# Kernel tuning notes

Hardware: AMD Instinct MI355X
Metric: run time of the kernel (lower is better)

The kernel has to match this reference:

```python
import jax, jax.numpy as jnp
import numpy as np
import math

NUM_WORDS = 8192
WORD_WIDTH = 512
PROJ_WIDTH = 64
NUM_HEADS = 8
SCALE_FACTOR = 100.0

def setup_inputs() -> dict:
    key = jax.random.key(0)
    kx, kq, kk, kv, ko = jax.random.split(key, 5)
    x = jax.random.normal(kx, (NUM_WORDS, WORD_WIDTH), dtype=jnp.float32)
    w_q = jax.random.normal(kq, (WORD_WIDTH, PROJ_WIDTH), dtype=jnp.float32) / SCALE_FACTOR
    w_k = jax.random.normal(kk, (WORD_WIDTH, PROJ_WIDTH), dtype=jnp.float32) / SCALE_FACTOR
    w_v = jax.random.normal(kv, (WORD_WIDTH, PROJ_WIDTH), dtype=jnp.float32) / SCALE_FACTOR
    w_o = jax.random.normal(ko, (WORD_WIDTH, WORD_WIDTH), dtype=jnp.float32)
    return {"x": x, "w_q": w_q, "w_k": w_k, "w_v": w_v, "w_o": w_o}

def reference(x, w_q, w_k, w_v, w_o):
    # Single self-attention head (all 8 heads in the source share the same weights).
    q = x @ w_q            # [N, P]
    k = x @ w_k            # [N, P]
    v = x @ w_v            # [N, P]
    scores = jax.nn.softmax((q @ k.T) / jnp.sqrt(jnp.float32(q.shape[1])), axis=1)  # [N, N]
    head = scores @ v      # [N, P]
    # concat of NUM_HEADS identical head outputs along dim=1
    concat = jnp.tile(head, (1, NUM_HEADS))  # [N, NUM_HEADS*P]
    return concat @ w_o    # [N, WORD_WIDTH]
```

## Files before the change

kernel.cpp:

```cpp
#include <hip/hip_runtime.h>
#include <stdint.h>

#define N_WORDS 8192
#define LOG2E_8 0.18033688011112043f

typedef __attribute__((ext_vector_type(8))) short short8;
typedef __attribute__((ext_vector_type(4))) float f32x4;
typedef __attribute__((ext_vector_type(2))) __fp16 pkhalf2;
typedef __attribute__((ext_vector_type(4))) _Float16 half4;
typedef __attribute__((ext_vector_type(8))) _Float16 half8;

__device__ __forceinline__ unsigned short f32_to_bf16(float f) {
    union { float f; unsigned u; } v; v.f = f;
    unsigned u = v.u;
    return (unsigned short)((u + 0x7FFFu + ((u >> 16) & 1u)) >> 16);
}

__device__ __forceinline__ unsigned short f32_to_f16(float f) {
    union { _Float16 h; unsigned short u; } cv;
    cv.h = (_Float16)f;
    return cv.u;
}

__device__ __forceinline__ void async16(const void* g, void* l) {
    __builtin_amdgcn_global_load_lds(
        (const __attribute__((address_space(1))) unsigned int*)g,
        (__attribute__((address_space(3))) unsigned int*)l, 16, 0, 0);
}

__global__ __launch_bounds__(256) void qkv_gemm(
    const float* __restrict__ x,
    const float* __restrict__ wq, const float* __restrict__ wk,
    const float* __restrict__ wv, const float* __restrict__ wo,
    unsigned short* __restrict__ qB, unsigned short* __restrict__ kB,
    unsigned short* __restrict__ vH, unsigned short* __restrict__ weT)
{
    int t = threadIdx.x;
    int mat = blockIdx.y;

    if (mat == 3) {
        int i = blockIdx.x * 256 + t;
        int p = i >> 9;
        int j = i & 511;
        float s = 0.0f;
#pragma unroll
        for (int h = 0; h < 8; ++h) s += wo[(size_t)(h * 64 + p) * 512 + j];
        weT[(size_t)j * 64 + p] = f32_to_f16(s);
        return;
    }

    __shared__ __align__(16) unsigned short ldsX[64 * 72];
    __shared__ __align__(16) unsigned short ldsW[64 * 72];

    int mt = blockIdx.x;
    const float* w = (mat == 0) ? wq : (mat == 1) ? wk : wv;

    int wvid = t >> 6, lane = t & 63;
    int lq = lane & 15, quad = lane >> 4;

    f32x4 acc[4];
#pragma unroll
    for (int nt = 0; nt < 4; ++nt) acc[nt] = (f32x4){0.f, 0.f, 0.f, 0.f};

    float4 xr[4];
    float wr[16];
    int wn = t & 63, wkbs = (t >> 6) * 16;

    {
        int k0 = 0;
#pragma unroll
        for (int j2 = 0; j2 < 4; ++j2) {
            int i = t + j2 * 256;
            int row = i >> 4, c4 = (i & 15) * 4;
            xr[j2] = *(const float4*)(x + (size_t)(mt * 64 + row) * 512 + k0 + c4);
        }
#pragma unroll
        for (int kk = 0; kk < 16; ++kk)
            wr[kk] = w[(size_t)(k0 + wkbs + kk) * 64 + wn];
    }

    for (int kb = 0; kb < 8; ++kb) {
        __syncthreads();
#pragma unroll
        for (int j2 = 0; j2 < 4; ++j2) {
            int i = t + j2 * 256;
            int row = i >> 4, c4 = (i & 15) * 4;
            unsigned p0 = f32_to_bf16(xr[j2].x) | ((unsigned)f32_to_bf16(xr[j2].y) << 16);
            unsigned p1 = f32_to_bf16(xr[j2].z) | ((unsigned)f32_to_bf16(xr[j2].w) << 16);
            *(uint2*)(&ldsX[row * 72 + c4]) = make_uint2(p0, p1);
        }
#pragma unroll
        for (int kk = 0; kk < 16; kk += 2) {
            unsigned p = f32_to_bf16(wr[kk]) | ((unsigned)f32_to_bf16(wr[kk + 1]) << 16);
            *(unsigned*)(&ldsW[wn * 72 + wkbs + kk]) = p;
        }
        __syncthreads();

        if (kb < 7) {
            int k0 = (kb + 1) * 64;
#pragma unroll
            for (int j2 = 0; j2 < 4; ++j2) {
                int i = t + j2 * 256;
                int row = i >> 4, c4 = (i & 15) * 4;
                xr[j2] = *(const float4*)(x + (size_t)(mt * 64 + row) * 512 + k0 + c4);
            }
#pragma unroll
            for (int kk = 0; kk < 16; ++kk)
                wr[kk] = w[(size_t)(k0 + wkbs + kk) * 64 + wn];
        }

        int m = wvid * 16 + lq;
        short8 a0 = *(const short8*)(&ldsX[m * 72 + quad * 8]);
        short8 a1 = *(const short8*)(&ldsX[m * 72 + 32 + quad * 8]);
#pragma unroll
        for (int nt = 0; nt < 4; ++nt) {
            short8 b0 = *(const short8*)(&ldsW[(nt * 16 + lq) * 72 + quad * 8]);
            short8 b1 = *(const short8*)(&ldsW[(nt * 16 + lq) * 72 + 32 + quad * 8]);
            acc[nt] = __builtin_amdgcn_mfma_f32_16x16x32_bf16(a0, b0, acc[nt], 0, 0, 0);
            acc[nt] = __builtin_amdgcn_mfma_f32_16x16x32_bf16(a1, b1, acc[nt], 0, 0, 0);
        }
    }

    int mrow_base = mt * 64 + wvid * 16;
#pragma unroll
    for (int nt = 0; nt < 4; ++nt) {
#pragma unroll
        for (int r = 0; r < 4; ++r) {
            int row = mrow_base + quad * 4 + r;
            int n = nt * 16 + lq;
            float v = acc[nt][r];
            if (mat == 0) {
                v *= LOG2E_8;
                int col = ((((n >> 3) ^ (row & 7)) << 3)) | (n & 7);
                qB[(size_t)row * 64 + col] = f32_to_bf16(v);
            } else if (mat == 1) {
                int col = ((((n >> 3) ^ (row & 7)) << 3)) | (n & 7);
                kB[(size_t)row * 64 + col] = f32_to_bf16(v);
            } else {
                int rs = (row & ~63) | (((((row >> 3) & 7) ^ (n & 7)) << 3)) | (row & 7);
                vH[(size_t)n * N_WORDS + rs] = f32_to_f16(v);
            }
        }
    }
}

__global__ __launch_bounds__(256) void attn_kernel(
    const unsigned short* __restrict__ qB,
    const unsigned short* __restrict__ kB,
    const unsigned short* __restrict__ vH,
    unsigned short* __restrict__ pOh, float* __restrict__ pl, int nk)
{
    __shared__ __align__(16) unsigned short ldsK[2][128 * 64];
    __shared__ __align__(16) unsigned short ldsV[2][64 * 128];

    int t = threadIdx.x;
    int wvid = t >> 6, lane = t & 63;
    int lq = lane & 15, quad = lane >> 4;
    int mbase = blockIdx.x * 128 + wvid * 32;
    int n0 = blockIdx.y * nk;

    short8 qf[2][2];
#pragma unroll
    for (int qs = 0; qs < 2; ++qs) {
        int row = mbase + qs * 16 + lq;
        const unsigned short* qr = qB + (size_t)row * 64;
        int s7 = row & 7;
        qf[qs][0] = *(const short8*)(qr + ((quad ^ s7) << 3));
        qf[qs][1] = *(const short8*)(qr + (((4 + quad) ^ s7) << 3));
    }

    f32x4 oacc[2][4];
#pragma unroll
    for (int qs = 0; qs < 2; ++qs)
#pragma unroll
        for (int vt = 0; vt < 4; ++vt) oacc[qs][vt] = (f32x4){0.f, 0.f, 0.f, 0.f};
    float lsum0 = 0.f, lsum1 = 0.f;

    auto stage = [&](int buf, int nb) {
        const char* gK = (const char*)kB + (size_t)nb * 128;
#pragma unroll
        for (int i = 0; i < 4; ++i) {
            int L0 = (wvid * 4 + i) * 64;
            async16(gK + (size_t)(L0 + lane) * 16, (char*)ldsK[buf] + (size_t)L0 * 16);
        }
#pragma unroll
        for (int i = 0; i < 4; ++i) {
            int L0 = (wvid * 4 + i) * 64;
            int L = L0 + lane;
            int vcol = L >> 4, ct = L & 15;
            const char* src = (const char*)vH + (size_t)vcol * 16384 +
                              (size_t)nb * 2 + ((ct >> 3) << 7) + ((ct & 7) << 4);
            async16(src, (char*)ldsV[buf] + (size_t)L0 * 16);
        }
    };

    int tiles = nk >> 7;
    stage(0, n0);
    int cur = 0;

    for (int tt = 0; tt < tiles; ++tt) {
        __syncthreads();
        if (tt + 1 < tiles) stage(cur ^ 1, n0 + (tt + 1) * 128);

        __builtin_amdgcn_s_setprio(1);
        const unsigned short* K = ldsK[cur];
        const unsigned short* V = ldsV[cur];

#pragma unroll
        for (int u = 0; u < 4; ++u) {
            f32x4 st[2][2];
#pragma unroll
            for (int h = 0; h < 2; ++h) {
                int nt = 2 * u + h;
                int s7 = lq & 7;
                const unsigned short* kr = K + (nt * 16 + lq) * 64;
                short8 a0 = *(const short8*)(kr + ((quad ^ s7) << 3));
                short8 a1 = *(const short8*)(kr + (((4 + quad) ^ s7) << 3));
                f32x4 s0 = (f32x4){0.f, 0.f, 0.f, 0.f};
                f32x4 s1 = (f32x4){0.f, 0.f, 0.f, 0.f};
                s0 = __builtin_amdgcn_mfma_f32_16x16x32_bf16(a0, qf[0][0], s0, 0, 0, 0);
                s0 = __builtin_amdgcn_mfma_f32_16x16x32_bf16(a1, qf[0][1], s0, 0, 0, 0);
                s1 = __builtin_amdgcn_mfma_f32_16x16x32_bf16(a0, qf[1][0], s1, 0, 0, 0);
                s1 = __builtin_amdgcn_mfma_f32_16x16x32_bf16(a1, qf[1][1], s1, 0, 0, 0);
                st[h][0] = s0;
                st[h][1] = s1;
            }

            union { half8 v8; pkhalf2 v2[4]; } pa[2];
#pragma unroll
            for (int h = 0; h < 2; ++h) {
                float e0 = exp2f(st[h][0][0]);
                float e1 = exp2f(st[h][0][1]);
                float e2 = exp2f(st[h][0][2]);
                float e3 = exp2f(st[h][0][3]);
                lsum0 += (e0 + e1) + (e2 + e3);
                pa[0].v2[h * 2 + 0] = __builtin_amdgcn_cvt_pkrtz(e0, e1);
                pa[0].v2[h * 2 + 1] = __builtin_amdgcn_cvt_pkrtz(e2, e3);
                float f0 = exp2f(st[h][1][0]);
                float f1 = exp2f(st[h][1][1]);
                float f2 = exp2f(st[h][1][2]);
                float f3 = exp2f(st[h][1][3]);
                lsum1 += (f0 + f1) + (f2 + f3);
                pa[1].v2[h * 2 + 0] = __builtin_amdgcn_cvt_pkrtz(f0, f1);
                pa[1].v2[h * 2 + 1] = __builtin_amdgcn_cvt_pkrtz(f2, f3);
            }

            int ct0 = 4 * u + (quad >> 1);
            int off = (quad & 1) * 4;
#pragma unroll
            for (int vt = 0; vt < 4; ++vt) {
                int vcol = vt * 16 + lq;
                int cs0 = (ct0 & 8) | ((ct0 & 7) ^ (vcol & 7));
                int ct1 = ct0 + 2;
                int cs1 = (ct1 & 8) | ((ct1 & 7) ^ (vcol & 7));
                union { half8 v8; half4 v4[2]; } vb;
                vb.v4[0] = *(const half4*)(V + vcol * 128 + (cs0 << 3) + off);
                vb.v4[1] = *(const half4*)(V + vcol * 128 + (cs1 << 3) + off);
                oacc[0][vt] = __builtin_amdgcn_mfma_f32_16x16x32_f16(
                    pa[0].v8, vb.v8, oacc[0][vt], 0, 0, 0);
                oacc[1][vt] = __builtin_amdgcn_mfma_f32_16x16x32_f16(
                    pa[1].v8, vb.v8, oacc[1][vt], 0, 0, 0);
            }
        }
        __builtin_amdgcn_s_setprio(0);
        cur ^= 1;
    }

    lsum0 += __shfl_xor(lsum0, 16); lsum0 += __shfl_xor(lsum0, 32);
    lsum1 += __shfl_xor(lsum1, 16); lsum1 += __shfl_xor(lsum1, 32);

    size_t obase = (size_t)blockIdx.y * N_WORDS;
    if (quad == 0) {
        pl[obase + mbase + lq] = lsum0;
        pl[obase + mbase + 16 + lq] = lsum1;
    }
#pragma unroll
    for (int qs = 0; qs < 2; ++qs)
#pragma unroll
        for (int vt = 0; vt < 4; ++vt)
#pragma unroll
            for (int r = 0; r < 4; ++r) {
                int row = mbase + qs * 16 + quad * 4 + r;
                pOh[(obase + row) * 64 + vt * 16 + lq] = f32_to_f16(oacc[qs][vt][r]);
            }
}

__global__ __launch_bounds__(256) void out_kernel(
    const unsigned short* __restrict__ pOh, const float* __restrict__ pl,
    const unsigned short* __restrict__ weT, float* __restrict__ out, int S)
{
    __shared__ __align__(16) _Float16 ldsH[16 * 72];
    int t = threadIdx.x;
    int r0 = blockIdx.x * 16;
    const _Float16* pOf = (const _Float16*)pOh;

#pragma unroll
    for (int j = 0; j < 4; ++j) {
        int i = t + j * 256;
        int row = i >> 6, d = i & 63;
        float so = 0.f, sl = 0.f;
        for (int s = 0; s < S; ++s) {
            so += (float)pOf[((size_t)s * N_WORDS + r0 + row) * 64 + d];
            sl += pl[(size_t)s * N_WORDS + r0 + row];
        }
        ldsH[row * 72 + d] = (_Float16)(so / sl);
    }
    __syncthreads();

    int wv = t >> 6, lane = t & 63;
    int lq = lane & 15, quad = lane >> 4;

    half8 a0 = *(const half8*)(&ldsH[lq * 72 + quad * 8]);
    half8 a1 = *(const half8*)(&ldsH[lq * 72 + 32 + quad * 8]);
    const _Float16* wT = (const _Float16*)weT;

#pragma unroll
    for (int ntl = 0; ntl < 8; ++ntl) {
        int nt = wv * 8 + ntl;
        const _Float16* wrow = wT + (size_t)(nt * 16 + lq) * 64;
        half8 b0 = *(const half8*)(wrow + quad * 8);
        half8 b1 = *(const half8*)(wrow + 32 + quad * 8);
        f32x4 acc = (f32x4){0.f, 0.f, 0.f, 0.f};
        acc = __builtin_amdgcn_mfma_f32_16x16x32_f16(a0, b0, acc, 0, 0, 0);
        acc = __builtin_amdgcn_mfma_f32_16x16x32_f16(a1, b1, acc, 0, 0, 0);
#pragma unroll
        for (int r = 0; r < 4; ++r)
            out[(size_t)(r0 + quad * 4 + r) * 512 + nt * 16 + lq] = acc[r];
    }
}

extern "C" void kernel_launch(void* const* d_in, const int* in_sizes, int n_in,
                              void* d_out, int out_size, void* d_ws, size_t ws_size,
                              hipStream_t stream)
{
    const float* x  = (const float*)d_in[0];
    const float* wq = (const float*)d_in[1];
    const float* wk = (const float*)d_in[2];
    const float* wv = (const float*)d_in[3];
    const float* wo = (const float*)d_in[4];
    float* out = (float*)d_out;

    char* ws = (char*)d_ws;
    unsigned short* qB  = (unsigned short*)(ws);
    unsigned short* kB  = (unsigned short*)(ws + 1048576);
    unsigned short* vH  = (unsigned short*)(ws + 2097152);
    unsigned short* weT = (unsigned short*)(ws + 3145728);
    float* pl           = (float*)(ws + 3211264);
    unsigned short* pOh = (unsigned short*)(ws + 3473408);

    int S = (ws_size >= (size_t)3473408 + 8u * 1048576u) ? 8 : 4;
    int nk = N_WORDS / S;

    hipLaunchKernelGGL(qkv_gemm, dim3(128, 4), dim3(256), 0, stream,
                       x, wq, wk, wv, wo, qB, kB, vH, weT);
    hipLaunchKernelGGL(attn_kernel, dim3(64, S), dim3(256), 0, stream,
                       qB, kB, vH, pOh, pl, nk);
    hipLaunchKernelGGL(out_kernel, dim3(512), dim3(256), 0, stream,
                       pOh, pl, weT, out, S);
}
```

Baseline: 130.3 us.

## Switch attention inner loop from 16x16x32 to 32x32x16 MFMA tiles

Rewrites the attention kernel's per-wave compute so that QK^T and PV use 32x32x16 MFMA instructions instead of 16x16x32. Q fragments, the K and V LDS read patterns, the softmax exponent packing and the output writeback are all remapped to the 32x32 register layout. Each wave now runs fewer, larger MFMAs, and each K/V fragment loaded from LDS feeds more math. The cost is larger 16-float accumulators and a changed LDS access pattern, which may raise register pressure or cause bank conflicts.

```diff
diff --git a/kernel.cpp b/kernel.cpp
--- a/kernel.cpp
+++ b/kernel.cpp
@@ -6,6 +6,7 @@
 
 typedef __attribute__((ext_vector_type(8))) short short8;
 typedef __attribute__((ext_vector_type(4))) float f32x4;
+typedef __attribute__((ext_vector_type(16))) float f32x16;
 typedef __attribute__((ext_vector_type(2))) __fp16 pkhalf2;
 typedef __attribute__((ext_vector_type(4))) _Float16 half4;
 typedef __attribute__((ext_vector_type(8))) _Float16 half8;
@@ -155,26 +156,27 @@
 
     int t = threadIdx.x;
     int wvid = t >> 6, lane = t & 63;
-    int lq = lane & 15, quad = lane >> 4;
+    int l31 = lane & 31, hi = lane >> 5;
     int mbase = blockIdx.x * 128 + wvid * 32;
     int n0 = blockIdx.y * nk;
 
-    short8 qf[2][2];
-#pragma unroll
-    for (int qs = 0; qs < 2; ++qs) {
-        int row = mbase + qs * 16 + lq;
-        const unsigned short* qr = qB + (size_t)row * 64;
-        int s7 = row & 7;
-        qf[qs][0] = *(const short8*)(qr + ((quad ^ s7) << 3));
-        qf[qs][1] = *(const short8*)(qr + (((4 + quad) ^ s7) << 3));
-    }
-
-    f32x4 oacc[2][4];
-#pragma unroll
-    for (int qs = 0; qs < 2; ++qs)
-#pragma unroll
-        for (int vt = 0; vt < 4; ++vt) oacc[qs][vt] = (f32x4){0.f, 0.f, 0.f, 0.f};
-    float lsum0 = 0.f, lsum1 = 0.f;
+    short8 qf[4];
+    {
+        int qrow = mbase + l31;
+        const unsigned short* qr = qB + (size_t)qrow * 64;
+        int s7 = qrow & 7;
+#pragma unroll
+        for (int c = 0; c < 4; ++c)
+            qf[c] = *(const short8*)(qr + (((2 * c + hi) ^ s7) << 3));
+    }
+
+    f32x16 zero16;
+#pragma unroll
+    for (int i = 0; i < 16; ++i) zero16[i] = 0.f;
+    f32x16 oacc[2];
+    oacc[0] = zero16;
+    oacc[1] = zero16;
+    float lsum = 0.f;
 
     auto stage = [&](int buf, int nb) {
         const char* gK = (const char*)kB + (size_t)nb * 128;
@@ -207,82 +209,58 @@
         const unsigned short* V = ldsV[cur];
 
 #pragma unroll
-        for (int u = 0; u < 4; ++u) {
-            f32x4 st[2][2];
-#pragma unroll
-            for (int h = 0; h < 2; ++h) {
-                int nt = 2 * u + h;
-                int s7 = lq & 7;
-                const unsigned short* kr = K + (nt * 16 + lq) * 64;
-                short8 a0 = *(const short8*)(kr + ((quad ^ s7) << 3));
-                short8 a1 = *(const short8*)(kr + (((4 + quad) ^ s7) << 3));
-                f32x4 s0 = (f32x4){0.f, 0.f, 0.f, 0.f};
-                f32x4 s1 = (f32x4){0.f, 0.f, 0.f, 0.f};
-                s0 = __builtin_amdgcn_mfma_f32_16x16x32_bf16(a0, qf[0][0], s0, 0, 0, 0);
-                s0 = __builtin_amdgcn_mfma_f32_16x16x32_bf16(a1, qf[0][1], s0, 0, 0, 0);
-                s1 = __builtin_amdgcn_mfma_f32_16x16x32_bf16(a0, qf[1][0], s1, 0, 0, 0);
-                s1 = __builtin_amdgcn_mfma_f32_16x16x32_bf16(a1, qf[1][1], s1, 0, 0, 0);
-                st[h][0] = s0;
-                st[h][1] = s1;
-            }
-
-            union { half8 v8; pkhalf2 v2[4]; } pa[2];
-#pragma unroll
-            for (int h = 0; h < 2; ++h) {
-                float e0 = exp2f(st[h][0][0]);
-                float e1 = exp2f(st[h][0][1]);
-                float e2 = exp2f(st[h][0][2]);
-                float e3 = exp2f(st[h][0][3]);
-                lsum0 += (e0 + e1) + (e2 + e3);
-                pa[0].v2[h * 2 + 0] = __builtin_amdgcn_cvt_pkrtz(e0, e1);
-                pa[0].v2[h * 2 + 1] = __builtin_amdgcn_cvt_pkrtz(e2, e3);
-                float f0 = exp2f(st[h][1][0]);
-                float f1 = exp2f(st[h][1][1]);
-                float f2 = exp2f(st[h][1][2]);
-                float f3 = exp2f(st[h][1][3]);
-                lsum1 += (f0 + f1) + (f2 + f3);
-                pa[1].v2[h * 2 + 0] = __builtin_amdgcn_cvt_pkrtz(f0, f1);
-                pa[1].v2[h * 2 + 1] = __builtin_amdgcn_cvt_pkrtz(f2, f3);
-            }
-
-            int ct0 = 4 * u + (quad >> 1);
-            int off = (quad & 1) * 4;
-#pragma unroll
-            for (int vt = 0; vt < 4; ++vt) {
-                int vcol = vt * 16 + lq;
-                int cs0 = (ct0 & 8) | ((ct0 & 7) ^ (vcol & 7));
-                int ct1 = ct0 + 2;
-                int cs1 = (ct1 & 8) | ((ct1 & 7) ^ (vcol & 7));
-                union { half8 v8; half4 v4[2]; } vb;
-                vb.v4[0] = *(const half4*)(V + vcol * 128 + (cs0 << 3) + off);
-                vb.v4[1] = *(const half4*)(V + vcol * 128 + (cs1 << 3) + off);
-                oacc[0][vt] = __builtin_amdgcn_mfma_f32_16x16x32_f16(
-                    pa[0].v8, vb.v8, oacc[0][vt], 0, 0, 0);
-                oacc[1][vt] = __builtin_amdgcn_mfma_f32_16x16x32_f16(
-                    pa[1].v8, vb.v8, oacc[1][vt], 0, 0, 0);
+        for (int nt = 0; nt < 4; ++nt) {
+            const unsigned short* kr = K + (nt * 32 + l31) * 64;
+            int s7 = l31 & 7;
+            f32x16 st = zero16;
+#pragma unroll
+            for (int c = 0; c < 4; ++c) {
+                short8 a = *(const short8*)(kr + (((2 * c + hi) ^ s7) << 3));
+                st = __builtin_amdgcn_mfma_f32_32x32x16_bf16(a, qf[c], st, 0, 0, 0);
+            }
+
+            union { half8 v8[2]; pkhalf2 v2[8]; } pa;
+#pragma unroll
+            for (int p = 0; p < 8; ++p) {
+                float e0 = exp2f(st[2 * p]);
+                float e1 = exp2f(st[2 * p + 1]);
+                lsum += e0 + e1;
+                pa.v2[p] = __builtin_amdgcn_cvt_pkrtz(e0, e1);
+            }
+
+#pragma unroll
+            for (int m = 0; m < 2; ++m) {
+                int c0 = 4 * nt + 2 * m;
+                int c1 = c0 + 1;
+#pragma unroll
+                for (int vt = 0; vt < 2; ++vt) {
+                    int vcol = vt * 32 + l31;
+                    int cs0 = (c0 & 8) | ((c0 & 7) ^ (vcol & 7));
+                    int cs1 = (c1 & 8) | ((c1 & 7) ^ (vcol & 7));
+                    union { half8 v8; half4 v4[2]; } vb;
+                    vb.v4[0] = *(const half4*)(V + vcol * 128 + (cs0 << 3) + hi * 4);
+                    vb.v4[1] = *(const half4*)(V + vcol * 128 + (cs1 << 3) + hi * 4);
+                    oacc[vt] = __builtin_amdgcn_mfma_f32_32x32x16_f16(
+                        pa.v8[m], vb.v8, oacc[vt], 0, 0, 0);
+                }
             }
         }
         __builtin_amdgcn_s_setprio(0);
         cur ^= 1;
     }
 
-    lsum0 += __shfl_xor(lsum0, 16); lsum0 += __shfl_xor(lsum0, 32);
-    lsum1 += __shfl_xor(lsum1, 16); lsum1 += __shfl_xor(lsum1, 32);
+    lsum += __shfl_xor(lsum, 32);
 
     size_t obase = (size_t)blockIdx.y * N_WORDS;
-    if (quad == 0) {
-        pl[obase + mbase + lq] = lsum0;
-        pl[obase + mbase + 16 + lq] = lsum1;
-    }
-#pragma unroll
-    for (int qs = 0; qs < 2; ++qs)
-#pragma unroll
-        for (int vt = 0; vt < 4; ++vt)
-#pragma unroll
-            for (int r = 0; r < 4; ++r) {
-                int row = mbase + qs * 16 + quad * 4 + r;
-                pOh[(obase + row) * 64 + vt * 16 + lq] = f32_to_f16(oacc[qs][vt][r]);
-            }
+    if (hi == 0) pl[obase + mbase + l31] = lsum;
+
+#pragma unroll
+    for (int vt = 0; vt < 2; ++vt)
+#pragma unroll
+        for (int r = 0; r < 16; ++r) {
+            int row = mbase + (r & 3) + 8 * (r >> 2) + 4 * hi;
+            pOh[(obase + row) * 64 + vt * 32 + l31] = f32_to_f16(oacc[vt][r]);
+        }
 }
 
 __global__ __launch_bounds__(256) void out_kernel(
```

Measured after the change: 131.0 us. About the same (+0.6%).
